# Performance work log

Hardware: AMD Instinct MI355X
Metric: run time of the kernel (lower is better)

The kernel has to match this reference:

```python
import jax, jax.numpy as jnp
import numpy as np

B, N, M, C = 8, 262144, 100, 7
BOX_WEIGHT = 2.0
EPS = 1e-7


def setup_inputs() -> dict:
    key = jax.random.key(0)
    k0, k1, k2, k3, k4, k5 = jax.random.split(key, 6)
    pred_cls = jax.random.normal(k0, (B, N, C), jnp.float32)
    pred_reg = jax.random.normal(k1, (B, N, 4), jnp.float32)
    anchors = jax.random.uniform(k2, (N, 2), jnp.float32) * 1024.0
    strides = jnp.ones((N,), jnp.float32) * 8.0
    ctr = jax.random.uniform(k3, (B, M, 2), jnp.float32) * 960.0 + 32.0
    wh = jax.random.uniform(k4, (B, M, 2), jnp.float32) * 120.0 + 8.0
    gt_boxes = jnp.concatenate([ctr - wh / 2, ctr + wh / 2], axis=-1)
    gt_labels = jax.random.randint(k5, (B, M), 1, C + 1)  # labels in [1, C]
    return {"pred_cls": pred_cls, "pred_reg": pred_reg, "anchors": anchors,
            "strides": strides, "gt_boxes": gt_boxes, "gt_labels": gt_labels}


def giou_loss(p, g):
    # p, g: (M,4) xyxy; elementwise GIoU loss = 1 - GIoU (torchvision semantics)
    ap = (p[:, 2] - p[:, 0]) * (p[:, 3] - p[:, 1])
    ag = (g[:, 2] - g[:, 0]) * (g[:, 3] - g[:, 1])
    lt = jnp.maximum(p[:, :2], g[:, :2])
    rb = jnp.minimum(p[:, 2:], g[:, 2:])
    whi = jnp.clip(rb - lt, 0.0)
    inter = whi[:, 0] * whi[:, 1]
    union = ap + ag - inter
    iou = inter / (union + EPS)
    ltc = jnp.minimum(p[:, :2], g[:, :2])
    rbc = jnp.maximum(p[:, 2:], g[:, 2:])
    whc = jnp.clip(rbc - ltc, 0.0)
    ac = whc[:, 0] * whc[:, 1]
    giou = iou - (ac - union) / (ac + EPS)
    return 1.0 - giou


def reference(pred_cls, pred_reg, anchors, strides, gt_boxes, gt_labels):
    num_anchors = anchors.shape[0]
    # head.decode_boxes: center+offset, exp size decode (guaranteed valid xyxy)
    s = strides[None, :, None]
    ctr = anchors[None] + pred_reg[..., :2] * s
    wh = jnp.exp(pred_reg[..., 2:]) * s
    pred_boxes = jnp.concatenate([ctr - wh / 2, ctr + wh / 2], axis=-1)  # (B,N,4)

    def per_image(cls_b, boxes_b, gt_b, lab_b):
        # nearest-anchor assignment via cdist (expanded as gemm to avoid (M,N,2))
        gc = (gt_b[:, :2] + gt_b[:, 2:]) / 2.0  # (M,2)
        d2 = (jnp.sum(gc * gc, -1)[:, None] + jnp.sum(anchors * anchors, -1)[None, :]
              - 2.0 * gc @ anchors.T)
        dist = jnp.sqrt(jnp.clip(d2, 0.0))  # (M,N)
        assigned = jnp.argmin(dist, axis=1)  # (M,)
        pos_mask = jnp.zeros((num_anchors,), bool).at[assigned].set(True)
        neg_mask = jnp.min(dist, axis=0) > 3.0
        # scatter one-hot class targets (collisions all set 1.0, order-free)
        cls_id = jnp.clip(lab_b - 1, 0, C - 1)
        tgt = jnp.zeros_like(cls_b).at[assigned, cls_id].set(1.0)
        # BCEWithLogits(mean) then scalar * sample_weight then .mean()  (faithful)
        bce_mean = jnp.mean(jnp.logaddexp(0.0, cls_b) - cls_b * tgt)
        sw = jnp.where(pos_mask, 2.0, 1.0) * jnp.where(neg_mask, 1.0, 0.1)
        loss_cls = bce_mean * jnp.mean(sw)
        # box loss: if #unique assigned anchors == M, original pairs boolean-masked
        # (anchor-index-sorted) preds with gt order; else gathers by assigned_idx
        lb_eq = jnp.mean(giou_loss(boxes_b[jnp.sort(assigned)], gt_b))
        lb_ne = jnp.mean(giou_loss(boxes_b[assigned], gt_b))
        loss_box = jnp.where(jnp.sum(pos_mask) == gt_b.shape[0], lb_eq, lb_ne)
        return loss_cls, loss_box

    lc, lb = jax.vmap(per_image)(pred_cls, pred_boxes, gt_boxes, gt_labels)
    total_cls = jnp.mean(lc)
    total_box = jnp.mean(lb)
    return total_cls + BOX_WEIGHT * total_box
```

## Files before the change

### kernel.cpp

```cpp
#include <hip/hip_runtime.h>

#define B_ 8
#define N_ 262144
#define M_ 100
#define C_ 7
#define EPSF 1e-7f
#define AB_ 2048
#define CH_ (N_ / AB_)
#define APT_ 8
#define SEG_ 4
#define SEGN_ (N_ / SEG_)

__device__ __forceinline__ float softplus0(float x) {
  return fmaxf(x, 0.0f) + log1pf(expf(-fabsf(x)));
}

__device__ __forceinline__ unsigned long long u64min(unsigned long long a,
                                                     unsigned long long b) {
  return b < a ? b : a;
}

__global__ void __launch_bounds__(256)
k_main(const float* __restrict__ pred_cls,
       const float* __restrict__ anchors,
       const float* __restrict__ gt_boxes,
       double* __restrict__ sp_sum,
       double* __restrict__ swb_sum,
       unsigned long long* __restrict__ part) {
  const int b = blockIdx.y;
  const int c = blockIdx.x;
  const int t = threadIdx.x;

  __shared__ float4 gt4[M_];
  __shared__ float red[256];
  __shared__ unsigned long long wb[M_][4];

  if (t < M_) {
    float4 g = reinterpret_cast<const float4*>(gt_boxes)[b * M_ + t];
    float gx = __fmul_rn(__fadd_rn(g.x, g.z), 0.5f);
    float gy = __fmul_rn(__fadd_rn(g.y, g.w), 0.5f);
    gt4[t] = make_float4(gx, gy, __fadd_rn(__fmul_rn(gx, gx), __fmul_rn(gy, gy)), 0.f);
  }

  const float4* pc = reinterpret_cast<const float4*>(
      pred_cls + (size_t)b * (size_t)(N_ * C_) + (size_t)c * (AB_ * C_));
  float acc_sp = 0.f;
  for (int k = 0; k < 14; ++k) {
    float4 v = pc[t + k * 256];
    acc_sp += softplus0(v.x) + softplus0(v.y) + softplus0(v.z) + softplus0(v.w);
  }
  red[t] = acc_sp;
  __syncthreads();
  for (int s = 128; s > 0; s >>= 1) {
    if (t < s) red[t] += red[t + s];
    __syncthreads();
  }
  if (t == 0) atomicAdd(&sp_sum[b], (double)red[0]);

  const int n0 = c * AB_;
  float ax[APT_], ay[APT_], t2[APT_], mind[APT_];
#pragma unroll
  for (int k = 0; k < APT_; ++k) {
    float2 a = reinterpret_cast<const float2*>(anchors)[n0 + t + k * 256];
    ax[k] = a.x; ay[k] = a.y;
    t2[k] = __fadd_rn(__fmul_rn(a.x, a.x), __fmul_rn(a.y, a.y));
    mind[k] = __int_as_float(0x7f800000);
  }
  __syncthreads();

  const int wid  = t >> 6;
  const int lane = t & 63;
  for (int m = 0; m < M_; ++m) {
    const float4 g = gt4[m];
    float bd = __int_as_float(0x7f800000);
    int bk = 0;
#pragma unroll
    for (int k = 0; k < APT_; ++k) {
      float dot = __fmaf_rn(g.y, ay[k], __fmul_rn(g.x, ax[k]));
      float d2  = __fsub_rn(__fadd_rn(g.z, t2[k]), __fadd_rn(dot, dot));
      d2 = fmaxf(d2, 0.0f);
      mind[k] = fminf(mind[k], d2);
      if (d2 < bd) { bd = d2; bk = k; }
    }
    unsigned bn = (unsigned)(n0 + t + (bk << 8));
    unsigned long long pk =
        ((unsigned long long)__float_as_uint(bd) << 32) | (unsigned long long)bn;
#pragma unroll
    for (int s = 1; s < 64; s <<= 1) {
      unsigned long long o = __shfl_xor((unsigned long long)pk, s, 64);
      pk = u64min(pk, o);
    }
    if (lane == 0) wb[m][wid] = pk;
  }
  __syncthreads();

  float accw = 0.f;
#pragma unroll
  for (int k = 0; k < APT_; ++k) accw += (sqrtf(mind[k]) > 3.0f) ? 1.0f : 0.1f;
  red[t] = accw;
  __syncthreads();
  for (int s = 128; s > 0; s >>= 1) {
    if (t < s) red[t] += red[t + s];
    __syncthreads();
  }
  if (t == 0) atomicAdd(&swb_sum[b], (double)red[0]);

  if (t < M_) {
    unsigned long long v = u64min(u64min(wb[t][0], wb[t][1]),
                                  u64min(wb[t][2], wb[t][3]));
    part[((size_t)(b * M_ + t)) * CH_ + c] = v;
  }
}

__global__ void __launch_bounds__(64)
k_amin2(const unsigned long long* __restrict__ part,
        unsigned long long* __restrict__ amin) {
  const int bm = blockIdx.x;
  const int t  = threadIdx.x;
  const unsigned long long* p = part + (size_t)bm * CH_;
  unsigned long long v = u64min(p[t], p[t + 64]);
#pragma unroll
  for (int s = 1; s < 64; s <<= 1)
    v = u64min(v, __shfl_xor((unsigned long long)v, s, 64));
  if (t == 0) amin[bm] = v;
}

__global__ void __launch_bounds__(256)
k_passA(const float* __restrict__ pred_cls,
        const float* __restrict__ anchors,
        const float* __restrict__ gt_boxes,
        double* __restrict__ sp_sum,
        double* __restrict__ swb_sum) {
  const int b = blockIdx.y;
  const int c = blockIdx.x;
  const int t = threadIdx.x;
  __shared__ float4 gt4[M_];
  __shared__ float red[256];
  if (t < M_) {
    float4 g = reinterpret_cast<const float4*>(gt_boxes)[b * M_ + t];
    float gx = __fmul_rn(__fadd_rn(g.x, g.z), 0.5f);
    float gy = __fmul_rn(__fadd_rn(g.y, g.w), 0.5f);
    gt4[t] = make_float4(gx, gy, __fadd_rn(__fmul_rn(gx, gx), __fmul_rn(gy, gy)), 0.f);
  }
  const float4* pc = reinterpret_cast<const float4*>(
      pred_cls + (size_t)b * (size_t)(N_ * C_) + (size_t)c * (1024 * C_));
  float acc_sp = 0.f;
#pragma unroll
  for (int k = 0; k < 7; ++k) {
    float4 v = pc[t + k * 256];
    acc_sp += softplus0(v.x) + softplus0(v.y) + softplus0(v.z) + softplus0(v.w);
  }
  red[t] = acc_sp;
  __syncthreads();
  for (int s = 128; s > 0; s >>= 1) {
    if (t < s) red[t] += red[t + s];
    __syncthreads();
  }
  if (t == 0) atomicAdd(&sp_sum[b], (double)red[0]);
  const int n0 = c * 1024;
  float ax[4], ay[4], t2[4], mind[4];
#pragma unroll
  for (int k = 0; k < 4; ++k) {
    float2 a = reinterpret_cast<const float2*>(anchors)[n0 + t + k * 256];
    ax[k] = a.x; ay[k] = a.y;
    t2[k] = __fadd_rn(__fmul_rn(a.x, a.x), __fmul_rn(a.y, a.y));
    mind[k] = __int_as_float(0x7f800000);
  }
#pragma unroll 2
  for (int m = 0; m < M_; ++m) {
    const float4 g = gt4[m];
#pragma unroll
    for (int k = 0; k < 4; ++k) {
      float dot = __fmaf_rn(g.y, ay[k], __fmul_rn(g.x, ax[k]));
      float d2  = __fsub_rn(__fadd_rn(g.z, t2[k]), __fadd_rn(dot, dot));
      mind[k] = fminf(mind[k], fmaxf(d2, 0.0f));
    }
  }
  float accw = 0.f;
#pragma unroll
  for (int k = 0; k < 4; ++k) accw += (sqrtf(mind[k]) > 3.0f) ? 1.0f : 0.1f;
  __syncthreads();
  red[t] = accw;
  __syncthreads();
  for (int s = 128; s > 0; s >>= 1) {
    if (t < s) red[t] += red[t + s];
    __syncthreads();
  }
  if (t == 0) atomicAdd(&swb_sum[b], (double)red[0]);
}

__global__ void __launch_bounds__(256)
k_argmin(const float* __restrict__ anchors,
         const float* __restrict__ gt_boxes,
         unsigned long long* __restrict__ amin) {
  const int bm  = blockIdx.y;
  const int seg = blockIdx.x;
  const float4 g = reinterpret_cast<const float4*>(gt_boxes)[bm];
  const float gx = __fmul_rn(__fadd_rn(g.x, g.z), 0.5f);
  const float gy = __fmul_rn(__fadd_rn(g.y, g.w), 0.5f);
  const float t1 = __fadd_rn(__fmul_rn(gx, gx), __fmul_rn(gy, gy));
  const float2* an = reinterpret_cast<const float2*>(anchors);
  float best = __int_as_float(0x7f800000);
  unsigned bestn = 0;
  const int n0 = seg * SEGN_;
#pragma unroll 4
  for (int n = n0 + threadIdx.x; n < n0 + SEGN_; n += 256) {
    float2 a = an[n];
    float t2  = __fadd_rn(__fmul_rn(a.x, a.x), __fmul_rn(a.y, a.y));
    float dot = __fmaf_rn(gy, a.y, __fmul_rn(gx, a.x));
    float d2  = __fsub_rn(__fadd_rn(t1, t2), __fadd_rn(dot, dot));
    d2 = fmaxf(d2, 0.0f);
    if (d2 < best) { best = d2; bestn = (unsigned)n; }
  }
  unsigned long long pk =
      ((unsigned long long)__float_as_uint(best) << 32) | (unsigned long long)bestn;
  __shared__ unsigned long long red[256];
  const int t = threadIdx.x;
  red[t] = pk;
  __syncthreads();
  for (int s = 128; s > 0; s >>= 1) {
    if (t < s) {
      unsigned long long o = red[t + s];
      if (o < red[t]) red[t] = o;
    }
    __syncthreads();
  }
  if (t == 0) atomicMin(&amin[bm], red[0]);
}

__global__ void __launch_bounds__(128)
k_final_img(const float* __restrict__ pred_cls,
            const float* __restrict__ pred_reg,
            const float* __restrict__ anchors,
            const float* __restrict__ strides,
            const float* __restrict__ gt_boxes,
            const int* __restrict__ gt_labels,
            const unsigned long long* __restrict__ amin,
            const double* __restrict__ sp_sum,
            const double* __restrict__ swb_sum,
            float* __restrict__ lc, float* __restrict__ lb) {
  const int b = blockIdx.x;
  const int t = threadIdx.x;
  __shared__ unsigned asg[M_];
  __shared__ int cid[M_];
  __shared__ unsigned srt[M_];
  __shared__ float4 gt4[M_];
  __shared__ float red[128];
  __shared__ int dupCount;
  if (t == 0) dupCount = 0;
  if (t < M_) {
    asg[t] = (unsigned)(amin[b * M_ + t] & 0xffffffffULL);
    int c = gt_labels[b * M_ + t] - 1;
    c = c < 0 ? 0 : (c > C_ - 1 ? C_ - 1 : c);
    cid[t] = c;
    float4 g = reinterpret_cast<const float4*>(gt_boxes)[b * M_ + t];
    float gx = __fmul_rn(__fadd_rn(g.x, g.z), 0.5f);
    float gy = __fmul_rn(__fadd_rn(g.y, g.w), 0.5f);
    gt4[t] = make_float4(gx, gy, __fadd_rn(__fmul_rn(gx, gx), __fmul_rn(gy, gy)), 0.f);
  }
  __syncthreads();

  float tg = 0.f, corr = 0.f;
  if (t < M_) {
    bool dupPair = false, dupIdx = false;
    for (int m = 0; m < t; ++m) {
      if (asg[m] == asg[t]) {
        dupIdx = true;
        if (cid[m] == cid[t]) dupPair = true;
      }
    }
    if (!dupPair) tg = pred_cls[((size_t)b * N_ + asg[t]) * C_ + cid[t]];
    if (dupIdx) atomicAdd(&dupCount, 1);
    if (!dupIdx) {
      float2 a = reinterpret_cast<const float2*>(anchors)[asg[t]];
      float t2 = __fadd_rn(__fmul_rn(a.x, a.x), __fmul_rn(a.y, a.y));
      float mind = __int_as_float(0x7f800000);
      for (int m = 0; m < M_; ++m) {
        float4 g = gt4[m];
        float dot = __fmaf_rn(g.y, a.y, __fmul_rn(g.x, a.x));
        float d2  = __fsub_rn(__fadd_rn(g.z, t2), __fadd_rn(dot, dot));
        mind = fminf(mind, fmaxf(d2, 0.0f));
      }
      corr = (sqrtf(mind) > 3.0f) ? 1.0f : 0.1f;
    }
  }
  red[t] = tg;
  __syncthreads();
  for (int s = 64; s > 0; s >>= 1) {
    if (t < s) red[t] += red[t + s];
    __syncthreads();
  }
  const float tgt_total = red[0];
  __syncthreads();
  red[t] = corr;
  __syncthreads();
  for (int s = 64; s > 0; s >>= 1) {
    if (t < s) red[t] += red[t + s];
    __syncthreads();
  }
  const float corr_total = red[0];
  const bool uniqueAll = (dupCount == 0);
  __syncthreads();

  if (uniqueAll && t < M_) {
    const unsigned v = asg[t];
    int rank = 0;
    for (int m = 0; m < M_; ++m) rank += (asg[m] < v) ? 1 : 0;
    srt[rank] = v;
  }
  __syncthreads();

  float gl = 0.f;
  if (t < M_) {
    const unsigned q = uniqueAll ? srt[t] : asg[t];
    float4 r = reinterpret_cast<const float4*>(pred_reg)[(size_t)b * N_ + q];
    float2 a = reinterpret_cast<const float2*>(anchors)[q];
    float s = strides[q];
    float cx = a.x + r.x * s, cy = a.y + r.y * s;
    float hx = (expf(r.z) * s) * 0.5f, hy = (expf(r.w) * s) * 0.5f;
    float px0 = cx - hx, py0 = cy - hy, px1 = cx + hx, py1 = cy + hy;
    float4 g = reinterpret_cast<const float4*>(gt_boxes)[b * M_ + t];
    float ap = (px1 - px0) * (py1 - py0);
    float ag = (g.z - g.x) * (g.w - g.y);
    float ltx = fmaxf(px0, g.x), lty = fmaxf(py0, g.y);
    float rbx = fminf(px1, g.z), rby = fminf(py1, g.w);
    float wix = fmaxf(rbx - ltx, 0.f), wiy = fmaxf(rby - lty, 0.f);
    float inter = wix * wiy;
    float uni = ap + ag - inter;
    float iou = inter / (uni + EPSF);
    float lcx = fminf(px0, g.x), lcy = fminf(py0, g.y);
    float rcx = fmaxf(px1, g.z), rcy = fmaxf(py1, g.w);
    float wcx = fmaxf(rcx - lcx, 0.f), wcy = fmaxf(rcy - lcy, 0.f);
    float ac = wcx * wcy;
    float giou = iou - (ac - uni) / (ac + EPSF);
    gl = 1.f - giou;
  }
  __syncthreads();
  red[t] = gl;
  __syncthreads();
  for (int s = 64; s > 0; s >>= 1) {
    if (t < s) red[t] += red[t + s];
    __syncthreads();
  }
  if (t == 0) {
    lb[b] = red[0] / (float)M_;
    float bce = (float)((sp_sum[b] - (double)tgt_total) / (double)(N_ * C_));
    float swm = (float)((swb_sum[b] + (double)corr_total) / (double)N_);
    lc[b] = bce * swm;
  }
}

__global__ void __launch_bounds__(64)
k_total(const float* __restrict__ lc, const float* __restrict__ lb,
        float* __restrict__ out) {
  if (threadIdx.x == 0 && blockIdx.x == 0) {
    float sc = 0.f, sb = 0.f;
    for (int b = 0; b < B_; ++b) { sc += lc[b]; sb += lb[b]; }
    out[0] = sc / 8.0f + 2.0f * (sb / 8.0f);
  }
}

extern "C" void kernel_launch(void* const* d_in, const int* in_sizes, int n_in,
                              void* d_out, int out_size, void* d_ws, size_t ws_size,
                              hipStream_t stream) {
  (void)in_sizes; (void)n_in; (void)out_size;
  const float* pred_cls  = (const float*)d_in[0];
  const float* pred_reg  = (const float*)d_in[1];
  const float* anchors   = (const float*)d_in[2];
  const float* strides   = (const float*)d_in[3];
  const float* gt_boxes  = (const float*)d_in[4];
  const int*   gt_labels = (const int*)d_in[5];
  float* out = (float*)d_out;

  char* ws = (char*)d_ws;
  double* sp_sum  = (double*)(ws);
  double* swb_sum = (double*)(ws + 64);

  const size_t part_off = 128;
  const size_t part_bytes = (size_t)B_ * M_ * CH_ * 8;
  const size_t amin_off = part_off + part_bytes;
  const size_t need = amin_off + 6400 + 64 + 64;

  if (ws_size >= need) {
    unsigned long long* part = (unsigned long long*)(ws + part_off);
    unsigned long long* amin = (unsigned long long*)(ws + amin_off);
    float* lc = (float*)(ws + amin_off + 6400);
    float* lb = (float*)(ws + amin_off + 6400 + 64);

    hipMemsetAsync(ws, 0, 128, stream);
    k_main<<<dim3(CH_, B_), dim3(256), 0, stream>>>(pred_cls, anchors, gt_boxes,
                                                    sp_sum, swb_sum, part);
    k_amin2<<<dim3(B_ * M_), dim3(64), 0, stream>>>(part, amin);
    k_final_img<<<dim3(B_), dim3(128), 0, stream>>>(pred_cls, pred_reg, anchors,
                                                    strides, gt_boxes, gt_labels,
                                                    amin, sp_sum, swb_sum, lc, lb);
    k_total<<<dim3(1), dim3(64), 0, stream>>>(lc, lb, out);
  } else {
    unsigned long long* amin = (unsigned long long*)(ws + 128);
    float* lc = (float*)(ws + 128 + 6400);
    float* lb = (float*)(ws + 128 + 6400 + 32);
    hipMemsetAsync(ws, 0, 128, stream);
    hipMemsetAsync(ws + 128, 0xFF, 6400, stream);
    k_passA<<<dim3(N_ / 1024, B_), dim3(256), 0, stream>>>(pred_cls, anchors, gt_boxes,
                                                           sp_sum, swb_sum);
    k_argmin<<<dim3(SEG_, B_ * M_), dim3(256), 0, stream>>>(anchors, gt_boxes, amin);
    k_final_img<<<dim3(B_), dim3(128), 0, stream>>>(pred_cls, pred_reg, anchors,
                                                    strides, gt_boxes, gt_labels,
                                                    amin, sp_sum, swb_sum, lc, lb);
    k_total<<<dim3(1), dim3(64), 0, stream>>>(lc, lb, out);
  }
}
```

Measured before the change: 258.3 us.

## Fuse argmin partial reduction into final kernel and streamline per-gt wave argmin

Result: faster. 249.5 us (-3.4%).

```diff
diff --git a/kernel.cpp b/kernel.cpp
--- a/kernel.cpp
+++ b/kernel.cpp
@@ -11,14 +11,13 @@
 #define SEG_ 4
 #define SEGN_ (N_ / SEG_)
 
+typedef unsigned long long ull;
+
 __device__ __forceinline__ float softplus0(float x) {
   return fmaxf(x, 0.0f) + log1pf(expf(-fabsf(x)));
 }
 
-__device__ __forceinline__ unsigned long long u64min(unsigned long long a,
-                                                     unsigned long long b) {
-  return b < a ? b : a;
-}
+__device__ __forceinline__ ull u64min(ull a, ull b) { return b < a ? b : a; }
 
 __global__ void __launch_bounds__(256)
 k_main(const float* __restrict__ pred_cls,
@@ -26,14 +25,14 @@
        const float* __restrict__ gt_boxes,
        double* __restrict__ sp_sum,
        double* __restrict__ swb_sum,
-       unsigned long long* __restrict__ part) {
+       ull* __restrict__ part) {
   const int b = blockIdx.y;
   const int c = blockIdx.x;
   const int t = threadIdx.x;
 
   __shared__ float4 gt4[M_];
   __shared__ float red[256];
-  __shared__ unsigned long long wb[M_][4];
+  __shared__ ull wb[M_][4];
 
   if (t < M_) {
     float4 g = reinterpret_cast<const float4*>(gt_boxes)[b * M_ + t];
@@ -59,35 +58,40 @@
 
   const int n0 = c * AB_;
   float ax[APT_], ay[APT_], t2[APT_], mind[APT_];
+  unsigned nn[APT_];
 #pragma unroll
   for (int k = 0; k < APT_; ++k) {
     float2 a = reinterpret_cast<const float2*>(anchors)[n0 + t + k * 256];
     ax[k] = a.x; ay[k] = a.y;
     t2[k] = __fadd_rn(__fmul_rn(a.x, a.x), __fmul_rn(a.y, a.y));
     mind[k] = __int_as_float(0x7f800000);
-  }
-  __syncthreads();
-
+    nn[k] = (unsigned)(n0 + t + (k << 8));
+  }
   const int wid  = t >> 6;
   const int lane = t & 63;
+  int bidx[6];
+#pragma unroll
+  for (int i = 0; i < 6; ++i) bidx[i] = ((lane ^ (1 << i)) << 2);
+  __syncthreads();
+
+#pragma unroll 2
   for (int m = 0; m < M_; ++m) {
     const float4 g = gt4[m];
-    float bd = __int_as_float(0x7f800000);
-    int bk = 0;
+    ull pk = 0xffffffffffffffffULL;
 #pragma unroll
     for (int k = 0; k < APT_; ++k) {
       float dot = __fmaf_rn(g.y, ay[k], __fmul_rn(g.x, ax[k]));
       float d2  = __fsub_rn(__fadd_rn(g.z, t2[k]), __fadd_rn(dot, dot));
       d2 = fmaxf(d2, 0.0f);
       mind[k] = fminf(mind[k], d2);
-      if (d2 < bd) { bd = d2; bk = k; }
-    }
-    unsigned bn = (unsigned)(n0 + t + (bk << 8));
-    unsigned long long pk =
-        ((unsigned long long)__float_as_uint(bd) << 32) | (unsigned long long)bn;
-#pragma unroll
-    for (int s = 1; s < 64; s <<= 1) {
-      unsigned long long o = __shfl_xor((unsigned long long)pk, s, 64);
+      ull cand = ((ull)__float_as_uint(d2) << 32) | (ull)nn[k];
+      pk = u64min(pk, cand);
+    }
+#pragma unroll
+    for (int i = 0; i < 6; ++i) {
+      int lo = __builtin_amdgcn_ds_bpermute(bidx[i], (int)(unsigned)(pk & 0xffffffffULL));
+      int hi = __builtin_amdgcn_ds_bpermute(bidx[i], (int)(unsigned)(pk >> 32));
+      ull o = ((ull)(unsigned)hi << 32) | (ull)(unsigned)lo;
       pk = u64min(pk, o);
     }
     if (lane == 0) wb[m][wid] = pk;
@@ -106,139 +110,22 @@
   if (t == 0) atomicAdd(&swb_sum[b], (double)red[0]);
 
   if (t < M_) {
-    unsigned long long v = u64min(u64min(wb[t][0], wb[t][1]),
-                                  u64min(wb[t][2], wb[t][3]));
+    ull v = u64min(u64min(wb[t][0], wb[t][1]), u64min(wb[t][2], wb[t][3]));
     part[((size_t)(b * M_ + t)) * CH_ + c] = v;
   }
 }
 
-__global__ void __launch_bounds__(64)
-k_amin2(const unsigned long long* __restrict__ part,
-        unsigned long long* __restrict__ amin) {
-  const int bm = blockIdx.x;
-  const int t  = threadIdx.x;
-  const unsigned long long* p = part + (size_t)bm * CH_;
-  unsigned long long v = u64min(p[t], p[t + 64]);
-#pragma unroll
-  for (int s = 1; s < 64; s <<= 1)
-    v = u64min(v, __shfl_xor((unsigned long long)v, s, 64));
-  if (t == 0) amin[bm] = v;
-}
-
-__global__ void __launch_bounds__(256)
-k_passA(const float* __restrict__ pred_cls,
-        const float* __restrict__ anchors,
-        const float* __restrict__ gt_boxes,
-        double* __restrict__ sp_sum,
-        double* __restrict__ swb_sum) {
-  const int b = blockIdx.y;
-  const int c = blockIdx.x;
-  const int t = threadIdx.x;
-  __shared__ float4 gt4[M_];
-  __shared__ float red[256];
-  if (t < M_) {
-    float4 g = reinterpret_cast<const float4*>(gt_boxes)[b * M_ + t];
-    float gx = __fmul_rn(__fadd_rn(g.x, g.z), 0.5f);
-    float gy = __fmul_rn(__fadd_rn(g.y, g.w), 0.5f);
-    gt4[t] = make_float4(gx, gy, __fadd_rn(__fmul_rn(gx, gx), __fmul_rn(gy, gy)), 0.f);
-  }
-  const float4* pc = reinterpret_cast<const float4*>(
-      pred_cls + (size_t)b * (size_t)(N_ * C_) + (size_t)c * (1024 * C_));
-  float acc_sp = 0.f;
-#pragma unroll
-  for (int k = 0; k < 7; ++k) {
-    float4 v = pc[t + k * 256];
-    acc_sp += softplus0(v.x) + softplus0(v.y) + softplus0(v.z) + softplus0(v.w);
-  }
-  red[t] = acc_sp;
-  __syncthreads();
-  for (int s = 128; s > 0; s >>= 1) {
-    if (t < s) red[t] += red[t + s];
-    __syncthreads();
-  }
-  if (t == 0) atomicAdd(&sp_sum[b], (double)red[0]);
-  const int n0 = c * 1024;
-  float ax[4], ay[4], t2[4], mind[4];
-#pragma unroll
-  for (int k = 0; k < 4; ++k) {
-    float2 a = reinterpret_cast<const float2*>(anchors)[n0 + t + k * 256];
-    ax[k] = a.x; ay[k] = a.y;
-    t2[k] = __fadd_rn(__fmul_rn(a.x, a.x), __fmul_rn(a.y, a.y));
-    mind[k] = __int_as_float(0x7f800000);
-  }
-#pragma unroll 2
-  for (int m = 0; m < M_; ++m) {
-    const float4 g = gt4[m];
-#pragma unroll
-    for (int k = 0; k < 4; ++k) {
-      float dot = __fmaf_rn(g.y, ay[k], __fmul_rn(g.x, ax[k]));
-      float d2  = __fsub_rn(__fadd_rn(g.z, t2[k]), __fadd_rn(dot, dot));
-      mind[k] = fminf(mind[k], fmaxf(d2, 0.0f));
-    }
-  }
-  float accw = 0.f;
-#pragma unroll
-  for (int k = 0; k < 4; ++k) accw += (sqrtf(mind[k]) > 3.0f) ? 1.0f : 0.1f;
-  __syncthreads();
-  red[t] = accw;
-  __syncthreads();
-  for (int s = 128; s > 0; s >>= 1) {
-    if (t < s) red[t] += red[t + s];
-    __syncthreads();
-  }
-  if (t == 0) atomicAdd(&swb_sum[b], (double)red[0]);
-}
-
-__global__ void __launch_bounds__(256)
-k_argmin(const float* __restrict__ anchors,
+__global__ void __launch_bounds__(128)
+k_final2(const float* __restrict__ pred_cls,
+         const float* __restrict__ pred_reg,
+         const float* __restrict__ anchors,
+         const float* __restrict__ strides,
          const float* __restrict__ gt_boxes,
-         unsigned long long* __restrict__ amin) {
-  const int bm  = blockIdx.y;
-  const int seg = blockIdx.x;
-  const float4 g = reinterpret_cast<const float4*>(gt_boxes)[bm];
-  const float gx = __fmul_rn(__fadd_rn(g.x, g.z), 0.5f);
-  const float gy = __fmul_rn(__fadd_rn(g.y, g.w), 0.5f);
-  const float t1 = __fadd_rn(__fmul_rn(gx, gx), __fmul_rn(gy, gy));
-  const float2* an = reinterpret_cast<const float2*>(anchors);
-  float best = __int_as_float(0x7f800000);
-  unsigned bestn = 0;
-  const int n0 = seg * SEGN_;
-#pragma unroll 4
-  for (int n = n0 + threadIdx.x; n < n0 + SEGN_; n += 256) {
-    float2 a = an[n];
-    float t2  = __fadd_rn(__fmul_rn(a.x, a.x), __fmul_rn(a.y, a.y));
-    float dot = __fmaf_rn(gy, a.y, __fmul_rn(gx, a.x));
-    float d2  = __fsub_rn(__fadd_rn(t1, t2), __fadd_rn(dot, dot));
-    d2 = fmaxf(d2, 0.0f);
-    if (d2 < best) { best = d2; bestn = (unsigned)n; }
-  }
-  unsigned long long pk =
-      ((unsigned long long)__float_as_uint(best) << 32) | (unsigned long long)bestn;
-  __shared__ unsigned long long red[256];
-  const int t = threadIdx.x;
-  red[t] = pk;
-  __syncthreads();
-  for (int s = 128; s > 0; s >>= 1) {
-    if (t < s) {
-      unsigned long long o = red[t + s];
-      if (o < red[t]) red[t] = o;
-    }
-    __syncthreads();
-  }
-  if (t == 0) atomicMin(&amin[bm], red[0]);
-}
-
-__global__ void __launch_bounds__(128)
-k_final_img(const float* __restrict__ pred_cls,
-            const float* __restrict__ pred_reg,
-            const float* __restrict__ anchors,
-            const float* __restrict__ strides,
-            const float* __restrict__ gt_boxes,
-            const int* __restrict__ gt_labels,
-            const unsigned long long* __restrict__ amin,
-            const double* __restrict__ sp_sum,
-            const double* __restrict__ swb_sum,
-            float* __restrict__ lc, float* __restrict__ lb) {
+         const int* __restrict__ gt_labels,
+         const ull* __restrict__ part,
+         const double* __restrict__ sp_sum,
+         const double* __restrict__ swb_sum,
+         float* __restrict__ lc, float* __restrict__ lb) {
   const int b = blockIdx.x;
   const int t = threadIdx.x;
   __shared__ unsigned asg[M_];
@@ -249,10 +136,18 @@
   __shared__ int dupCount;
   if (t == 0) dupCount = 0;
   if (t < M_) {
-    asg[t] = (unsigned)(amin[b * M_ + t] & 0xffffffffULL);
-    int c = gt_labels[b * M_ + t] - 1;
-    c = c < 0 ? 0 : (c > C_ - 1 ? C_ - 1 : c);
-    cid[t] = c;
+    const ull* p = part + ((size_t)(b * M_ + t)) * CH_;
+    ull v0 = 0xffffffffffffffffULL, v1 = v0, v2 = v0, v3 = v0;
+    for (int c = 0; c < CH_; c += 4) {
+      v0 = u64min(v0, p[c]);
+      v1 = u64min(v1, p[c + 1]);
+      v2 = u64min(v2, p[c + 2]);
+      v3 = u64min(v3, p[c + 3]);
+    }
+    asg[t] = (unsigned)(u64min(u64min(v0, v1), u64min(v2, v3)) & 0xffffffffULL);
+    int cc = gt_labels[b * M_ + t] - 1;
+    cc = cc < 0 ? 0 : (cc > C_ - 1 ? C_ - 1 : cc);
+    cid[t] = cc;
     float4 g = reinterpret_cast<const float4*>(gt_boxes)[b * M_ + t];
     float gx = __fmul_rn(__fadd_rn(g.x, g.z), 0.5f);
     float gy = __fmul_rn(__fadd_rn(g.y, g.w), 0.5f);
@@ -350,6 +245,230 @@
   }
 }
 
+__global__ void __launch_bounds__(256)
+k_passA(const float* __restrict__ pred_cls,
+        const float* __restrict__ anchors,
+        const float* __restrict__ gt_boxes,
+        double* __restrict__ sp_sum,
+        double* __restrict__ swb_sum) {
+  const int b = blockIdx.y;
+  const int c = blockIdx.x;
+  const int t = threadIdx.x;
+  __shared__ float4 gt4[M_];
+  __shared__ float red[256];
+  if (t < M_) {
+    float4 g = reinterpret_cast<const float4*>(gt_boxes)[b * M_ + t];
+    float gx = __fmul_rn(__fadd_rn(g.x, g.z), 0.5f);
+    float gy = __fmul_rn(__fadd_rn(g.y, g.w), 0.5f);
+    gt4[t] = make_float4(gx, gy, __fadd_rn(__fmul_rn(gx, gx), __fmul_rn(gy, gy)), 0.f);
+  }
+  const float4* pc = reinterpret_cast<const float4*>(
+      pred_cls + (size_t)b * (size_t)(N_ * C_) + (size_t)c * (1024 * C_));
+  float acc_sp = 0.f;
+#pragma unroll
+  for (int k = 0; k < 7; ++k) {
+    float4 v = pc[t + k * 256];
+    acc_sp += softplus0(v.x) + softplus0(v.y) + softplus0(v.z) + softplus0(v.w);
+  }
+  red[t] = acc_sp;
+  __syncthreads();
+  for (int s = 128; s > 0; s >>= 1) {
+    if (t < s) red[t] += red[t + s];
+    __syncthreads();
+  }
+  if (t == 0) atomicAdd(&sp_sum[b], (double)red[0]);
+  const int n0 = c * 1024;
+  float ax[4], ay[4], t2[4], mind[4];
+#pragma unroll
+  for (int k = 0; k < 4; ++k) {
+    float2 a = reinterpret_cast<const float2*>(anchors)[n0 + t + k * 256];
+    ax[k] = a.x; ay[k] = a.y;
+    t2[k] = __fadd_rn(__fmul_rn(a.x, a.x), __fmul_rn(a.y, a.y));
+    mind[k] = __int_as_float(0x7f800000);
+  }
+#pragma unroll 2
+  for (int m = 0; m < M_; ++m) {
+    const float4 g = gt4[m];
+#pragma unroll
+    for (int k = 0; k < 4; ++k) {
+      float dot = __fmaf_rn(g.y, ay[k], __fmul_rn(g.x, ax[k]));
+      float d2  = __fsub_rn(__fadd_rn(g.z, t2[k]), __fadd_rn(dot, dot));
+      mind[k] = fminf(mind[k], fmaxf(d2, 0.0f));
+    }
+  }
+  float accw = 0.f;
+#pragma unroll
+  for (int k = 0; k < 4; ++k) accw += (sqrtf(mind[k]) > 3.0f) ? 1.0f : 0.1f;
+  __syncthreads();
+  red[t] = accw;
+  __syncthreads();
+  for (int s = 128; s > 0; s >>= 1) {
+    if (t < s) red[t] += red[t + s];
+    __syncthreads();
+  }
+  if (t == 0) atomicAdd(&swb_sum[b], (double)red[0]);
+}
+
+__global__ void __launch_bounds__(256)
+k_argmin(const float* __restrict__ anchors,
+         const float* __restrict__ gt_boxes,
+         ull* __restrict__ amin) {
+  const int bm  = blockIdx.y;
+  const int seg = blockIdx.x;
+  const float4 g = reinterpret_cast<const float4*>(gt_boxes)[bm];
+  const float gx = __fmul_rn(__fadd_rn(g.x, g.z), 0.5f);
+  const float gy = __fmul_rn(__fadd_rn(g.y, g.w), 0.5f);
+  const float t1 = __fadd_rn(__fmul_rn(gx, gx), __fmul_rn(gy, gy));
+  const float2* an = reinterpret_cast<const float2*>(anchors);
+  float best = __int_as_float(0x7f800000);
+  unsigned bestn = 0;
+  const int n0 = seg * SEGN_;
+#pragma unroll 4
+  for (int n = n0 + threadIdx.x; n < n0 + SEGN_; n += 256) {
+    float2 a = an[n];
+    float t2  = __fadd_rn(__fmul_rn(a.x, a.x), __fmul_rn(a.y, a.y));
+    float dot = __fmaf_rn(gy, a.y, __fmul_rn(gx, a.x));
+    float d2  = __fsub_rn(__fadd_rn(t1, t2), __fadd_rn(dot, dot));
+    d2 = fmaxf(d2, 0.0f);
+    if (d2 < best) { best = d2; bestn = (unsigned)n; }
+  }
+  ull pk = ((ull)__float_as_uint(best) << 32) | (ull)bestn;
+  __shared__ ull red[256];
+  const int t = threadIdx.x;
+  red[t] = pk;
+  __syncthreads();
+  for (int s = 128; s > 0; s >>= 1) {
+    if (t < s) {
+      ull o = red[t + s];
+      if (o < red[t]) red[t] = o;
+    }
+    __syncthreads();
+  }
+  if (t == 0) atomicMin(&amin[bm], red[0]);
+}
+
+__global__ void __launch_bounds__(128)
+k_final_img(const float* __restrict__ pred_cls,
+            const float* __restrict__ pred_reg,
+            const float* __restrict__ anchors,
+            const float* __restrict__ strides,
+            const float* __restrict__ gt_boxes,
+            const int* __restrict__ gt_labels,
+            const ull* __restrict__ amin,
+            const double* __restrict__ sp_sum,
+            const double* __restrict__ swb_sum,
+            float* __restrict__ lc, float* __restrict__ lb) {
+  const int b = blockIdx.x;
+  const int t = threadIdx.x;
+  __shared__ unsigned asg[M_];
+  __shared__ int cid[M_];
+  __shared__ unsigned srt[M_];
+  __shared__ float4 gt4[M_];
+  __shared__ float red[128];
+  __shared__ int dupCount;
+  if (t == 0) dupCount = 0;
+  if (t < M_) {
+    asg[t] = (unsigned)(amin[b * M_ + t] & 0xffffffffULL);
+    int c = gt_labels[b * M_ + t] - 1;
+    c = c < 0 ? 0 : (c > C_ - 1 ? C_ - 1 : c);
+    cid[t] = c;
+    float4 g = reinterpret_cast<const float4*>(gt_boxes)[b * M_ + t];
+    float gx = __fmul_rn(__fadd_rn(g.x, g.z), 0.5f);
+    float gy = __fmul_rn(__fadd_rn(g.y, g.w), 0.5f);
+    gt4[t] = make_float4(gx, gy, __fadd_rn(__fmul_rn(gx, gx), __fmul_rn(gy, gy)), 0.f);
+  }
+  __syncthreads();
+
+  float tg = 0.f, corr = 0.f;
+  if (t < M_) {
+    bool dupPair = false, dupIdx = false;
+    for (int m = 0; m < t; ++m) {
+      if (asg[m] == asg[t]) {
+        dupIdx = true;
+        if (cid[m] == cid[t]) dupPair = true;
+      }
+    }
+    if (!dupPair) tg = pred_cls[((size_t)b * N_ + asg[t]) * C_ + cid[t]];
+    if (dupIdx) atomicAdd(&dupCount, 1);
+    if (!dupIdx) {
+      float2 a = reinterpret_cast<const float2*>(anchors)[asg[t]];
+      float t2 = __fadd_rn(__fmul_rn(a.x, a.x), __fmul_rn(a.y, a.y));
+      float mind = __int_as_float(0x7f800000);
+      for (int m = 0; m < M_; ++m) {
+        float4 g = gt4[m];
+        float dot = __fmaf_rn(g.y, a.y, __fmul_rn(g.x, a.x));
+        float d2  = __fsub_rn(__fadd_rn(g.z, t2), __fadd_rn(dot, dot));
+        mind = fminf(mind, fmaxf(d2, 0.0f));
+      }
+      corr = (sqrtf(mind) > 3.0f) ? 1.0f : 0.1f;
+    }
+  }
+  red[t] = tg;
+  __syncthreads();
+  for (int s = 64; s > 0; s >>= 1) {
+    if (t < s) red[t] += red[t + s];
+    __syncthreads();
+  }
+  const float tgt_total = red[0];
+  __syncthreads();
+  red[t] = corr;
+  __syncthreads();
+  for (int s = 64; s > 0; s >>= 1) {
+    if (t < s) red[t] += red[t + s];
+    __syncthreads();
+  }
+  const float corr_total = red[0];
+  const bool uniqueAll = (dupCount == 0);
+  __syncthreads();
+
+  if (uniqueAll && t < M_) {
+    const unsigned v = asg[t];
+    int rank = 0;
+    for (int m = 0; m < M_; ++m) rank += (asg[m] < v) ? 1 : 0;
+    srt[rank] = v;
+  }
+  __syncthreads();
+
+  float gl = 0.f;
+  if (t < M_) {
+    const unsigned q = uniqueAll ? srt[t] : asg[t];
+    float4 r = reinterpret_cast<const float4*>(pred_reg)[(size_t)b * N_ + q];
+    float2 a = reinterpret_cast<const float2*>(anchors)[q];
+    float s = strides[q];
+    float cx = a.x + r.x * s, cy = a.y + r.y * s;
+    float hx = (expf(r.z) * s) * 0.5f, hy = (expf(r.w) * s) * 0.5f;
+    float px0 = cx - hx, py0 = cy - hy, px1 = cx + hx, py1 = cy + hy;
+    float4 g = reinterpret_cast<const float4*>(gt_boxes)[b * M_ + t];
+    float ap = (px1 - px0) * (py1 - py0);
+    float ag = (g.z - g.x) * (g.w - g.y);
+    float ltx = fmaxf(px0, g.x), lty = fmaxf(py0, g.y);
+    float rbx = fminf(px1, g.z), rby = fminf(py1, g.w);
+    float wix = fmaxf(rbx - ltx, 0.f), wiy = fmaxf(rby - lty, 0.f);
+    float inter = wix * wiy;
+    float uni = ap + ag - inter;
+    float iou = inter / (uni + EPSF);
+    float lcx = fminf(px0, g.x), lcy = fminf(py0, g.y);
+    float rcx = fmaxf(px1, g.z), rcy = fmaxf(py1, g.w);
+    float wcx = fmaxf(rcx - lcx, 0.f), wcy = fmaxf(rcy - lcy, 0.f);
+    float ac = wcx * wcy;
+    float giou = iou - (ac - uni) / (ac + EPSF);
+    gl = 1.f - giou;
+  }
+  __syncthreads();
+  red[t] = gl;
+  __syncthreads();
+  for (int s = 64; s > 0; s >>= 1) {
+    if (t < s) red[t] += red[t + s];
+    __syncthreads();
+  }
+  if (t == 0) {
+    lb[b] = red[0] / (float)M_;
+    float bce = (float)((sp_sum[b] - (double)tgt_total) / (double)(N_ * C_));
+    float swm = (float)((swb_sum[b] + (double)corr_total) / (double)N_);
+    lc[b] = bce * swm;
+  }
+}
+
 __global__ void __launch_bounds__(64)
 k_total(const float* __restrict__ lc, const float* __restrict__ lb,
         float* __restrict__ out) {
@@ -378,25 +497,23 @@
 
   const size_t part_off = 128;
   const size_t part_bytes = (size_t)B_ * M_ * CH_ * 8;
-  const size_t amin_off = part_off + part_bytes;
-  const size_t need = amin_off + 6400 + 64 + 64;
+  const size_t tail_off = part_off + part_bytes;
+  const size_t need = tail_off + 64 + 64;
 
   if (ws_size >= need) {
-    unsigned long long* part = (unsigned long long*)(ws + part_off);
-    unsigned long long* amin = (unsigned long long*)(ws + amin_off);
-    float* lc = (float*)(ws + amin_off + 6400);
-    float* lb = (float*)(ws + amin_off + 6400 + 64);
+    ull* part = (ull*)(ws + part_off);
+    float* lc = (float*)(ws + tail_off);
+    float* lb = (float*)(ws + tail_off + 64);
 
     hipMemsetAsync(ws, 0, 128, stream);
     k_main<<<dim3(CH_, B_), dim3(256), 0, stream>>>(pred_cls, anchors, gt_boxes,
                                                     sp_sum, swb_sum, part);
-    k_amin2<<<dim3(B_ * M_), dim3(64), 0, stream>>>(part, amin);
-    k_final_img<<<dim3(B_), dim3(128), 0, stream>>>(pred_cls, pred_reg, anchors,
-                                                    strides, gt_boxes, gt_labels,
-                                                    amin, sp_sum, swb_sum, lc, lb);
+    k_final2<<<dim3(B_), dim3(128), 0, stream>>>(pred_cls, pred_reg, anchors,
+                                                 strides, gt_boxes, gt_labels,
+                                                 part, sp_sum, swb_sum, lc, lb);
     k_total<<<dim3(1), dim3(64), 0, stream>>>(lc, lb, out);
   } else {
-    unsigned long long* amin = (unsigned long long*)(ws + 128);
+    ull* amin = (ull*)(ws + 128);
     float* lc = (float*)(ws + 128 + 6400);
     float* lb = (float*)(ws + 128 + 6400 + 32);
     hipMemsetAsync(ws, 0, 128, stream);
```
